# Kernel optimization log

Measured on AMD Instinct MI355X. Metric: run time of the kernel, lower is better.

The kernel has to match this reference:

```python
import jax, jax.numpy as jnp
import numpy as np

HIDDEN = 2048
N_HEADS = 16
N_KV = 2
HEAD_DIM = 256
PARTIAL = 0.25
ROT = int(HEAD_DIM * PARTIAL)  # 64
BATCH, SEQ = 1, 4096
NEG = -1e9


def apply_partial_rope(x, cos, sin):
    # x: (b, s, h, d); rotate first ROT dims (rotate-half convention), pass rest through.
    x_rot, x_pass = x[..., :ROT], x[..., ROT:]
    half = ROT // 2
    x1, x2 = x_rot[..., :half], x_rot[..., half:]
    c = cos[None, :, None, :]  # (1, s, 1, rot/2)
    s = sin[None, :, None, :]
    rotated = jnp.concatenate([x1 * c - x2 * s, x1 * s + x2 * c], axis=-1)
    return jnp.concatenate([rotated, x_pass], axis=-1)


def setup_inputs() -> dict:
    key = jax.random.key(0)
    ks = jax.random.split(key, 6)
    hidden_states = jax.random.normal(ks[0], (BATCH, SEQ, HIDDEN), dtype=jnp.float32)
    # RoPE tables: theta = 10000^{-2i/rot}
    inv_freq = 1.0 / (10000.0 ** (np.arange(0, ROT, 2, dtype=np.float32) / ROT))
    ang = np.arange(SEQ, dtype=np.float32)[:, None] * inv_freq[None, :]  # (s, rot/2)
    cos = jnp.asarray(np.cos(ang))
    sin = jnp.asarray(np.sin(ang))
    # causal mask (1,1,s,s)
    mask = jnp.triu(jnp.full((SEQ, SEQ), NEG, dtype=jnp.float32), k=1)[None, None]
    scale = 0.02
    wq = jax.random.normal(ks[1], (HIDDEN, N_HEADS * HEAD_DIM), dtype=jnp.float32) * scale
    wk = jax.random.normal(ks[2], (HIDDEN, N_KV * HEAD_DIM), dtype=jnp.float32) * scale
    wv = jax.random.normal(ks[3], (HIDDEN, N_KV * HEAD_DIM), dtype=jnp.float32) * scale
    wo = jax.random.normal(ks[4], (N_HEADS * HEAD_DIM, HIDDEN), dtype=jnp.float32) * scale
    return {"hidden_states": hidden_states, "cos": cos, "sin": sin,
            "attention_mask": mask, "wq": wq, "wk": wk, "wv": wv, "wo": wo}


def reference(hidden_states, cos, sin, attention_mask, wq, wk, wv, wo):
    b, s, _ = hidden_states.shape
    g = N_HEADS // N_KV
    scale = HEAD_DIM ** -0.5
    q = (hidden_states @ wq).reshape(b, s, N_HEADS, HEAD_DIM)
    k = (hidden_states @ wk).reshape(b, s, N_KV, HEAD_DIM)
    v = (hidden_states @ wv).reshape(b, s, N_KV, HEAD_DIM)
    q = apply_partial_rope(q, cos, sin)
    k = apply_partial_rope(k, cos, sin)
    new_k, new_v = k, v  # kv cache (no prior cache)
    # GQA without repeat_interleave: group q heads by their kv head.
    # repeat_interleave maps q head h -> kv head h // g, matching this reshape.
    qg = q.reshape(b, s, N_KV, g, HEAD_DIM)
    scores = jnp.einsum('bqkgd,blkd->bkgql', qg, k) * scale  # (b, kv, g, s, s)
    scores = scores + attention_mask[:, :, None]  # broadcast (b,1,1,s,s)
    probs = jax.nn.softmax(scores.astype(jnp.float32), axis=-1).astype(q.dtype)
    ctx = jnp.einsum('bkgql,blkd->bqkgd', probs, v)  # (b, s, kv, g, d)
    attn_out = ctx.reshape(b, s, N_HEADS * HEAD_DIM)
    output = attn_out @ wo
    return output, new_k, new_v
```

## Files before the change

kernel.cpp:

```cpp
#include <hip/hip_runtime.h>
#include <hip/hip_bf16.h>

typedef __bf16 bf16;
typedef bf16 bf16x8 __attribute__((ext_vector_type(8)));
typedef bf16 bf16x4 __attribute__((ext_vector_type(4)));
typedef float f32x4 __attribute__((ext_vector_type(4)));

#define SEQ    4096
#define HIDDEN 2048
#define NHEADS 16
#define NKV    2
#define HDIM   256
#define ROTD   64
#define ROTH   32
#define QN     (NHEADS*HDIM)
#define KVN    (NKV*HDIM)

typedef __attribute__((address_space(3))) unsigned int lds_u32;
typedef const __attribute__((address_space(1))) unsigned int glb_u32;
__device__ __forceinline__ void async_copy16(const void* g, void* l) {
  __builtin_amdgcn_global_load_lds((glb_u32*)g, (lds_u32*)l, 16, 0, 0);
}

__global__ __launch_bounds__(256) void convert_f32_bf16(
    const float* __restrict__ in, bf16* __restrict__ out, int n)
{
  int i = (blockIdx.x * 256 + threadIdx.x) * 4;
  if (i >= n) return;
  f32x4 v = *(const f32x4*)(in + i);
  bf16x4 o;
  #pragma unroll
  for (int j = 0; j < 4; j++) o[j] = (bf16)v[j];
  *(bf16x4*)(out + i) = o;
}

template<typename T>
__global__ __launch_bounds__(256) void transpose_to_bf16(
    const T* __restrict__ in, bf16* __restrict__ out, int R, int C)
{
  __shared__ float tile[32][33];
  int bx = blockIdx.x * 32;
  int by = blockIdx.y * 32;
  int tx = threadIdx.x & 31, ty = threadIdx.x >> 5;
  #pragma unroll
  for (int i = 0; i < 4; i++)
    tile[ty + i*8][tx] = (float)in[(size_t)(by + ty + i*8) * C + bx + tx];
  __syncthreads();
  #pragma unroll
  for (int i = 0; i < 4; i++)
    out[(size_t)(bx + ty + i*8) * R + by + tx] = (bf16)tile[tx][ty + i*8];
}

template<bool WF32, bool WBF16>
__global__ __launch_bounds__(256) void gemm_bt(
    const bf16* __restrict__ A, const bf16* __restrict__ Bt,
    float* __restrict__ Cf, bf16* __restrict__ Cb,
    int M, int N, int K)
{
  const int bm = blockIdx.y * 128;
  const int bn = blockIdx.x * 128;
  const int tid = threadIdx.x;
  const int wave = tid >> 6, lane = tid & 63;
  const int l16 = lane & 15, quad = lane >> 4;
  const int wr = (wave & 1) * 64;
  const int wc = (wave >> 1) * 64;

  __shared__ bf16 As[128*32];
  __shared__ bf16 Bs[128*32];

  f32x4 acc[4][4];
  #pragma unroll
  for (int r = 0; r < 4; r++)
    #pragma unroll
    for (int c = 0; c < 4; c++) acc[r][c] = (f32x4){0.f,0.f,0.f,0.f};

  const int arow = tid >> 2;
  const int acol = (tid & 3) * 8;
  const bf16* ag0 = A  + (size_t)(bm + arow)      * K + acol;
  const bf16* ag1 = A  + (size_t)(bm + 64 + arow) * K + acol;
  const bf16* bg0 = Bt + (size_t)(bn + arow)      * K + acol;
  const bf16* bg1 = Bt + (size_t)(bn + 64 + arow) * K + acol;
  bf16* la = As + tid*8;
  bf16* lb = Bs + tid*8;

  for (int kk = 0; kk < K; kk += 32) {
    __syncthreads();
    async_copy16(ag0 + kk, la);
    async_copy16(ag1 + kk, la + 2048);
    async_copy16(bg0 + kk, lb);
    async_copy16(bg1 + kk, lb + 2048);
    __syncthreads();

    bf16x8 af[4], bfr[4];
    #pragma unroll
    for (int r = 0; r < 4; r++) af[r]  = *(const bf16x8*)&As[(wr + r*16 + l16)*32 + quad*8];
    #pragma unroll
    for (int c = 0; c < 4; c++) bfr[c] = *(const bf16x8*)&Bs[(wc + c*16 + l16)*32 + quad*8];
    #pragma unroll
    for (int r = 0; r < 4; r++)
      #pragma unroll
      for (int c = 0; c < 4; c++)
        acc[r][c] = __builtin_amdgcn_mfma_f32_16x16x32_bf16(af[r], bfr[c], acc[r][c], 0, 0, 0);
  }

  #pragma unroll
  for (int r = 0; r < 4; r++)
    #pragma unroll
    for (int c = 0; c < 4; c++)
      #pragma unroll
      for (int rr = 0; rr < 4; rr++) {
        size_t idx = (size_t)(bm + wr + r*16 + quad*4 + rr) * N + bn + wc + c*16 + l16;
        if (WF32)  Cf[idx] = acc[r][c][rr];
        if (WBF16) Cb[idx] = (bf16)acc[r][c][rr];
      }
}

#define G256_STG(gp, stride, lbase, b, h, kt) do {                            \
    async_copy16((gp) + (size_t)((h)*128     ) * (stride) + (size_t)(kt)*64,  \
                 (lbase) + (b)*16384 + (h)*8192);                             \
    async_copy16((gp) + (size_t)((h)*128 + 64) * (stride) + (size_t)(kt)*64,  \
                 (lbase) + (b)*16384 + (h)*8192 + 4096);                      \
  } while (0)

#define G256_DSA(b, P) do {                                                   \
    _Pragma("unroll")                                                         \
    for (int m2 = 0; m2 < 2; m2++) {                                          \
      const int ro = (b)*16384 + arow0 + ((P)*2 + m2) * 1024;                 \
      af[m2][0] = *(const bf16x8*)&smem[ro + fc0];                            \
      af[m2][1] = *(const bf16x8*)&smem[ro + fc1];                            \
    }                                                                         \
  } while (0)

#define G256_DSB(b) do {                                                      \
    _Pragma("unroll")                                                         \
    for (int n4 = 0; n4 < 4; n4++) {                                          \
      const int ro = 32768 + (b)*16384 + brow0 + n4 * 1024;                   \
      bq[n4][0] = *(const bf16x8*)&smem[ro + fc0];                            \
      bq[n4][1] = *(const bf16x8*)&smem[ro + fc1];                            \
    }                                                                         \
  } while (0)

#define G256_MM(P) do {                                                       \
    _Pragma("unroll")                                                         \
    for (int m2 = 0; m2 < 2; m2++)                                            \
      _Pragma("unroll")                                                       \
      for (int n4 = 0; n4 < 4; n4++) {                                        \
        acc[(P)*2+m2][n4] = __builtin_amdgcn_mfma_f32_16x16x32_bf16(          \
            af[m2][0], bq[n4][0], acc[(P)*2+m2][n4], 0, 0, 0);                \
        acc[(P)*2+m2][n4] = __builtin_amdgcn_mfma_f32_16x16x32_bf16(          \
            af[m2][1], bq[n4][1], acc[(P)*2+m2][n4], 0, 0, 0);                \
      }                                                                       \
  } while (0)

#define G256_BAR  __builtin_amdgcn_s_barrier()
#define G256_WLG  do { asm volatile("s_waitcnt lgkmcnt(0)" ::: "memory");     \
                       __builtin_amdgcn_sched_barrier(0); } while (0)

template<bool WF32, bool WBF16>
__global__ __launch_bounds__(512, 2) void gemm256(
    const bf16* __restrict__ A, const bf16* __restrict__ Bt,
    float* __restrict__ Cf0, float* __restrict__ Cf1, bf16* __restrict__ Cb,
    int N, int K, int lda, int ldb)
{
  const int gx = gridDim.x;
  const int nwg = gx * gridDim.y;
  int wg = blockIdx.y * gx + blockIdx.x;
  wg = (wg & 7) * (nwg >> 3) + (wg >> 3);
  const int bn = (wg % gx) * 256;
  const int bm = (wg / gx) * 256;

  const int z = blockIdx.z;
  A  += (size_t)z * K;
  Bt += (size_t)z * K;
  float* __restrict__ Cf = z ? Cf1 : Cf0;

  const int tid = threadIdx.x;
  const int lane = tid & 63;
  const int l16 = lane & 15, quad = lane >> 4;
  const int wv = tid >> 6;
  const int wm = wv >> 2;
  const int wn = wv & 3;

  __shared__ bf16 smem[65536];

  const int srow = tid >> 3;
  const int scol = ((tid & 7) ^ (srow & 7)) << 3;
  const bf16* Ag = A  + (size_t)(bm + srow) * lda + scol;
  const bf16* Bg = Bt + (size_t)(bn + srow) * ldb + scol;
  bf16* lA = smem + tid * 8;
  bf16* lB = smem + 32768 + tid * 8;

  const int fsw = l16 & 7;
  const int fc0 = ((quad       ^ fsw) << 3);
  const int fc1 = (((4 + quad) ^ fsw) << 3);
  const int arow0 = (wm * 128 + l16) * 64;
  const int brow0 = (wn * 64  + l16) * 64;

  f32x4 acc[8][4];
  #pragma unroll
  for (int m = 0; m < 8; m++)
    #pragma unroll
    for (int n = 0; n < 4; n++) acc[m][n] = (f32x4){0.f,0.f,0.f,0.f};

  const int niter = K >> 7;

  G256_STG(Ag, lda, lA, 0, 0, 0);  G256_STG(Ag, lda, lA, 0, 1, 0);
  G256_STG(Bg, ldb, lB, 0, 0, 0);  G256_STG(Bg, ldb, lB, 0, 1, 0);
  G256_STG(Bg, ldb, lB, 1, 0, 1);  G256_STG(Bg, ldb, lB, 1, 1, 1);
  asm volatile("s_waitcnt vmcnt(4)" ::: "memory");
  G256_BAR;

  bf16x8 af[2][2];
  bf16x8 bq[4][2];

  for (int i = 0; i < niter; i++) {
    const int O = 2*i + 1;
    const bool nl = (i + 1 < niter);

    G256_DSB(0); G256_DSA(0, 0);
    G256_STG(Ag, lda, lA, 1, 0, O);
    G256_BAR; G256_WLG;
    __builtin_amdgcn_s_setprio(1); G256_MM(0); __builtin_amdgcn_s_setprio(0);
    G256_BAR;
    G256_DSA(0, 1);
    G256_STG(Ag, lda, lA, 1, 1, O);
    G256_BAR; G256_WLG;
    __builtin_amdgcn_s_setprio(1); G256_MM(1); __builtin_amdgcn_s_setprio(0);
    G256_BAR;
    G256_DSA(0, 2);
    if (nl) G256_STG(Bg, ldb, lB, 0, 0, O+1);
    G256_BAR; G256_WLG;
    __builtin_amdgcn_s_setprio(1); G256_MM(2); __builtin_amdgcn_s_setprio(0);
    G256_BAR;
    G256_DSA(0, 3);
    if (nl) G256_STG(Bg, ldb, lB, 0, 1, O+1);
    G256_BAR; G256_WLG;
    __builtin_amdgcn_s_setprio(1); G256_MM(3); __builtin_amdgcn_s_setprio(0);
    if (nl) asm volatile("s_waitcnt vmcnt(4)" ::: "memory");
    else    asm volatile("s_waitcnt vmcnt(0)" ::: "memory");
    G256_BAR;
    G256_DSB(1); G256_DSA(1, 0);
    if (nl) G256_STG(Ag, lda, lA, 0, 0, O+1);
    G256_BAR; G256_WLG;
    __builtin_amdgcn_s_setprio(1); G256_MM(0); __builtin_amdgcn_s_setprio(0);
    G256_BAR;
    G256_DSA(1, 1);
    if (nl) G256_STG(Ag, lda, lA, 0, 1, O+1);
    G256_BAR; G256_WLG;
    __builtin_amdgcn_s_setprio(1); G256_MM(1); __builtin_amdgcn_s_setprio(0);
    G256_BAR;
    G256_DSA(1, 2);
    if (nl) G256_STG(Bg, ldb, lB, 1, 0, O+2);
    G256_BAR; G256_WLG;
    __builtin_amdgcn_s_setprio(1); G256_MM(2); __builtin_amdgcn_s_setprio(0);
    G256_BAR;
    G256_DSA(1, 3);
    if (nl) G256_STG(Bg, ldb, lB, 1, 1, O+2);
    G256_BAR; G256_WLG;
    __builtin_amdgcn_s_setprio(1); G256_MM(3); __builtin_amdgcn_s_setprio(0);
    if (nl) asm volatile("s_waitcnt vmcnt(4)" ::: "memory");
    G256_BAR;
  }

  #pragma unroll
  for (int mf = 0; mf < 8; mf++)
    #pragma unroll
    for (int n = 0; n < 4; n++)
      #pragma unroll
      for (int rr = 0; rr < 4; rr++) {
        size_t idx = (size_t)(bm + wm*128 + mf*16 + quad*4 + rr) * N
                   + bn + wn*64 + n*16 + l16;
        if (WF32)  Cf[idx] = acc[mf][n][rr];
        if (WBF16) Cb[idx] = (bf16)acc[mf][n][rr];
      }
}

__global__ __launch_bounds__(256) void add_f32(
    const float* __restrict__ a, float* __restrict__ b, int n)
{
  int i = (blockIdx.x * 256 + threadIdx.x) * 4;
  if (i >= n) return;
  f32x4 x = *(const f32x4*)(a + i);
  f32x4 y = *(const f32x4*)(b + i);
  #pragma unroll
  for (int j = 0; j < 4; j++) y[j] += x[j];
  *(f32x4*)(b + i) = y;
}

__global__ __launch_bounds__(256) void rope_kernel(
    bf16* __restrict__ Q, bf16* __restrict__ K,
    const float* __restrict__ cosb, const float* __restrict__ sinb,
    float* __restrict__ newk)
{
  int s = blockIdx.x;
  int t = threadIdx.x;
  __shared__ float cf[ROTH], sf[ROTH];
  if (t < ROTH) { cf[t] = cosb[s*ROTH + t]; sf[t] = sinb[s*ROTH + t]; }
  __syncthreads();

  float qv[4];
  #pragma unroll
  for (int i = 0; i < 4; i++) {
    int w = t + 256*i;
    int h = w >> 6, d = w & 63;
    size_t base = ((size_t)s*NHEADS + h)*HDIM;
    if (d < ROTH) {
      float x1 = (float)Q[base + d], x2 = (float)Q[base + d + ROTH];
      qv[i] = x1*cf[d] - x2*sf[d];
    } else {
      int dd = d - ROTH;
      float x1 = (float)Q[base + dd], x2 = (float)Q[base + d];
      qv[i] = x1*sf[dd] + x2*cf[dd];
    }
  }
  float kvv[2];
  #pragma unroll
  for (int i = 0; i < 2; i++) {
    int w = t + 256*i;
    int h = w >> 8, d = w & 255;
    size_t base = ((size_t)s*NKV + h)*HDIM;
    if (d < ROTH) {
      kvv[i] = (float)K[base + d]*cf[d] - (float)K[base + d + ROTH]*sf[d];
    } else if (d < ROTD) {
      int dd = d - ROTH;
      kvv[i] = (float)K[base + dd]*sf[dd] + (float)K[base + d]*cf[dd];
    } else {
      kvv[i] = (float)K[base + d];
    }
  }
  __syncthreads();
  #pragma unroll
  for (int i = 0; i < 4; i++) {
    int w = t + 256*i;
    int h = w >> 6, d = w & 63;
    Q[((size_t)s*NHEADS + h)*HDIM + d] = (bf16)qv[i];
  }
  #pragma unroll
  for (int i = 0; i < 2; i++) {
    int w = t + 256*i;
    int h = w >> 8, d = w & 255;
    size_t base = ((size_t)s*NKV + h)*HDIM;
    K[base + d]    = (bf16)kvv[i];
    newk[base + d] = kvv[i];
  }
}

__global__ __launch_bounds__(256, 2) void attn_v6(
    const bf16* __restrict__ Q, const bf16* __restrict__ Kc,
    const bf16* __restrict__ Vt, bf16* __restrict__ ctx)
{
  const int d = blockIdx.y * gridDim.x + blockIdx.x;
  const int r = (d < 256) ? d : 767 - d;
  const int qs = 31 - (r >> 4);
  const int h  = r & 15, kvh = h >> 3;
  const int tid = threadIdx.x, wave = tid >> 6, lane = tid & 63;
  const int l16 = lane & 15, quad = lane >> 4;
  const int q0 = qs*128 + wave*32;

  __shared__ bf16 Ks[2][32*256];
  __shared__ bf16 Vs[2][256*32];
  __shared__ bf16 PsAll[4][32][40];
  bf16 (*Ps)[40] = PsAll[wave];

  bf16x8 aq[2][8];
  #pragma unroll
  for (int u = 0; u < 2; u++) {
    const bf16* qp = Q + (size_t)(q0 + u*16 + l16)*QN + h*HDIM + quad*8;
    #pragma unroll
    for (int c = 0; c < 8; c++) aq[u][c] = *(const bf16x8*)(qp + c*32);
  }

  f32x4 o[2][16];
  #pragma unroll
  for (int u = 0; u < 2; u++)
    #pragma unroll
    for (int c = 0; c < 16; c++) o[u][c] = (f32x4){0.f,0.f,0.f,0.f};
  float lsum[2][4] = {{0.f,0.f,0.f,0.f},{0.f,0.f,0.f,0.f}};

  const int krow0 = tid >> 5;
  const int kcg   = ((tid & 31) ^ (krow0 & 7)) * 8;
  const bf16* kg  = Kc + (size_t)kvh*HDIM + kcg;
  const int vd0 = tid >> 2;
  const int vcg = ((tid & 3) ^ (vd0 & 3)) * 8;
  const bf16* vg  = Vt + (size_t)(kvh*HDIM + vd0)*SEQ + vcg;

  const int ntiles = qs*4 + 4;

  #define ATTN_STAGE(t, b) do {                                               \
    const int _l0 = (t)*32;                                                   \
    bf16* _ks = &Ks[b][0] + tid*8;                                            \
    bf16* _vs = &Vs[b][0] + tid*8;                                            \
    _Pragma("unroll")                                                         \
    for (int p = 0; p < 4; p++) {                                             \
      async_copy16(kg + (size_t)(_l0 + p*8 + krow0)*KVN, _ks + p*2048);       \
      async_copy16(vg + (size_t)(p*64)*SEQ + _l0,        _vs + p*2048);       \
    }                                                                         \
  } while (0)

  ATTN_STAGE(0, 0);
  ATTN_STAGE(1, 1);
  asm volatile("s_waitcnt vmcnt(8)" ::: "memory");
  __builtin_amdgcn_s_barrier();

  for (int t = 0; t < ntiles; t++) {
    const int b  = t & 1;
    const int l0 = t*32;

    if (l0 <= q0 + 31) {
      f32x4 s[2][2];
      #pragma unroll
      for (int u = 0; u < 2; u++)
        #pragma unroll
        for (int t4 = 0; t4 < 2; t4++) s[u][t4] = (f32x4){0.f,0.f,0.f,0.f};
      #pragma unroll
      for (int c = 0; c < 8; c++) {
        const int cs = ((c*4 + quad) ^ (l16 & 7)) * 8;
        #pragma unroll
        for (int t4 = 0; t4 < 2; t4++) {
          bf16x8 kb = *(const bf16x8*)&Ks[b][(t4*16 + l16)*256 + cs];
          #pragma unroll
          for (int u = 0; u < 2; u++)
            s[u][t4] = __builtin_amdgcn_mfma_f32_16x16x32_bf16(aq[u][c], kb, s[u][t4], 0, 0, 0);
        }
      }

      const bool need_mask = (l0 + 31 > q0);
      #pragma unroll
      for (int u = 0; u < 2; u++)
        #pragma unroll
        for (int rr = 0; rr < 4; rr++) {
          const int row = q0 + u*16 + quad*4 + rr;
          float p0 = __expf(fmaf(s[u][0][rr], 0.0625f, -12.0f));
          float p1 = __expf(fmaf(s[u][1][rr], 0.0625f, -12.0f));
          if (need_mask) {
            if (l0 +      l16 > row) p0 = 0.f;
            if (l0 + 16 + l16 > row) p1 = 0.f;
          }
          lsum[u][rr] += p0 + p1;
          Ps[u*16 + quad*4 + rr][l16]      = (bf16)p0;
          Ps[u*16 + quad*4 + rr][16 + l16] = (bf16)p1;
        }

      bf16x8 pa[2];
      #pragma unroll
      for (int u = 0; u < 2; u++) pa[u] = *(const bf16x8*)&Ps[u*16 + l16][quad*8];
      #pragma unroll
      for (int c = 0; c < 16; c++) {
        const int vs = ((quad ^ (l16 & 3))) * 8;
        bf16x8 vb = *(const bf16x8*)&Vs[b][(c*16 + l16)*32 + vs];
        #pragma unroll
        for (int u = 0; u < 2; u++)
          o[u][c] = __builtin_amdgcn_mfma_f32_16x16x32_bf16(pa[u], vb, o[u][c], 0, 0, 0);
      }
    }

    if (t + 1 < ntiles) {
      __builtin_amdgcn_s_barrier();
      if (t + 2 < ntiles) {
        ATTN_STAGE(t + 2, b);
        asm volatile("s_waitcnt vmcnt(8)" ::: "memory");
      } else {
        asm volatile("s_waitcnt vmcnt(0)" ::: "memory");
      }
      __builtin_amdgcn_s_barrier();
    }
  }
  #undef ATTN_STAGE

  #pragma unroll
  for (int u = 0; u < 2; u++)
    #pragma unroll
    for (int rr = 0; rr < 4; rr++) {
      float l = lsum[u][rr];
      l += __shfl_xor(l, 1);
      l += __shfl_xor(l, 2);
      l += __shfl_xor(l, 4);
      l += __shfl_xor(l, 8);
      float inv = 1.0f / l;
      size_t base = (size_t)(q0 + u*16 + quad*4 + rr)*QN + h*HDIM;
      #pragma unroll
      for (int c = 0; c < 16; c++)
        ctx[base + c*16 + l16] = (bf16)(o[u][c][rr] * inv);
    }
}

extern "C" void kernel_launch(void* const* d_in, const int* in_sizes, int n_in,
                              void* d_out, int out_size, void* d_ws, size_t ws_size,
                              hipStream_t stream)
{
  const float* X    = (const float*)d_in[0];
  const float* cosb = (const float*)d_in[1];
  const float* sinb = (const float*)d_in[2];
  const float* wq   = (const float*)d_in[4];
  const float* wk   = (const float*)d_in[5];
  const float* wv   = (const float*)d_in[6];
  const float* wo   = (const float*)d_in[7];

  float* out  = (float*)d_out;
  float* newk = out  + (size_t)SEQ*HIDDEN;
  float* newv = newk + (size_t)SEQ*KVN;

  bf16* Xb  = (bf16*)d_ws;
  bf16* wqT = Xb  + (size_t)SEQ*HIDDEN;
  bf16* Qb  = wqT + (size_t)QN*HIDDEN;
  bf16* Kb  = Qb  + (size_t)SEQ*QN;
  bf16* Vb  = Kb  + (size_t)SEQ*KVN;
  bf16* Vt  = Vb  + (size_t)SEQ*KVN;
  bf16* wkT = Vt  + (size_t)KVN*SEQ;
  bf16* wvT = wkT + (size_t)KVN*HIDDEN;
  bf16* woT = wvT + (size_t)KVN*HIDDEN;
  bf16* ctx = Xb;
  float* part = (float*)Qb;

  dim3 blk(256);
  convert_f32_bf16<<<dim3(SEQ*HIDDEN/1024), blk, 0, stream>>>(X, Xb, SEQ*HIDDEN);
  transpose_to_bf16<float><<<dim3(QN/32,     HIDDEN/32), blk, 0, stream>>>(wq, wqT, HIDDEN, QN);
  transpose_to_bf16<float><<<dim3(KVN/32,    HIDDEN/32), blk, 0, stream>>>(wk, wkT, HIDDEN, KVN);
  transpose_to_bf16<float><<<dim3(KVN/32,    HIDDEN/32), blk, 0, stream>>>(wv, wvT, HIDDEN, KVN);
  transpose_to_bf16<float><<<dim3(HIDDEN/32, QN/32),     blk, 0, stream>>>(wo, woT, QN, HIDDEN);

  gemm256<false,true><<<dim3(QN/256, SEQ/256, 1), dim3(512), 0, stream>>>(
      Xb, wqT, nullptr, nullptr, Qb, QN, HIDDEN, HIDDEN, HIDDEN);
  gemm_bt<false,true><<<dim3(KVN/128, SEQ/128), blk, 0, stream>>>(Xb, wkT, nullptr, Kb, SEQ, KVN, HIDDEN);
  gemm_bt<true, true><<<dim3(KVN/128, SEQ/128), blk, 0, stream>>>(Xb, wvT, newv,   Vb, SEQ, KVN, HIDDEN);

  rope_kernel<<<dim3(SEQ), blk, 0, stream>>>(Qb, Kb, cosb, sinb, newk);
  transpose_to_bf16<bf16><<<dim3(KVN/32, SEQ/32), blk, 0, stream>>>(Vb, Vt, SEQ, KVN);

  attn_v6<<<dim3(SEQ/128, NHEADS), blk, 0, stream>>>(Qb, Kb, Vt, ctx);

  gemm256<true,false><<<dim3(HIDDEN/256, SEQ/256, 2), dim3(512), 0, stream>>>(
      ctx, woT, out, part, nullptr, HIDDEN, QN/2, QN, QN);
  add_f32<<<dim3(SEQ*HIDDEN/1024), blk, 0, stream>>>(part, out, SEQ*HIDDEN);
}
```

Baseline: 722.6 us.

## Share K/V tiles across two heads per 512-thread attention block with 64-key tiles

The attention kernel now runs 8 waves per block covering two query heads that share one KV head, so each K/V tile loaded into LDS serves twice as many query rows. Key tiles grow from 32 to 64 rows and each is processed in two 32-key halves. It also switches exp to exp2 with a folded scale constant and raises wave priority around the MFMA loops. The aim is to halve global K/V traffic and the number of barriers per key, at the cost of larger LDS use (64KB+), lower occupancy per block, and dropping the heavy-first load-balancing block order.

```diff
diff --git a/kernel.cpp b/kernel.cpp
--- a/kernel.cpp
+++ b/kernel.cpp
@@ -345,21 +345,21 @@
   }
 }
 
-__global__ __launch_bounds__(256, 2) void attn_v6(
+__global__ __launch_bounds__(512, 2) void attn_v7(
     const bf16* __restrict__ Q, const bf16* __restrict__ Kc,
     const bf16* __restrict__ Vt, bf16* __restrict__ ctx)
 {
-  const int d = blockIdx.y * gridDim.x + blockIdx.x;
-  const int r = (d < 256) ? d : 767 - d;
-  const int qs = 31 - (r >> 4);
-  const int h  = r & 15, kvh = h >> 3;
+  const int qs  = blockIdx.x;
+  const int hp  = blockIdx.y;
+  const int kvh = hp >> 2;
   const int tid = threadIdx.x, wave = tid >> 6, lane = tid & 63;
   const int l16 = lane & 15, quad = lane >> 4;
-  const int q0 = qs*128 + wave*32;
-
-  __shared__ bf16 Ks[2][32*256];
-  __shared__ bf16 Vs[2][256*32];
-  __shared__ bf16 PsAll[4][32][40];
+  const int h   = hp*2 + (wave >> 2);
+  const int q0  = qs*128 + (wave & 3)*32;
+
+  __shared__ bf16 Ks[2][64*256];
+  __shared__ bf16 Vs[2][256*64];
+  __shared__ bf16 PsAll[8][32][40];
   bf16 (*Ps)[40] = PsAll[wave];
 
   bf16x8 aq[2][8];
@@ -380,20 +380,20 @@
   const int krow0 = tid >> 5;
   const int kcg   = ((tid & 31) ^ (krow0 & 7)) * 8;
   const bf16* kg  = Kc + (size_t)kvh*HDIM + kcg;
-  const int vd0 = tid >> 2;
-  const int vcg = ((tid & 3) ^ (vd0 & 3)) * 8;
+  const int vd0 = tid >> 3;
+  const int vcg = ((tid & 7) ^ (vd0 & 7)) * 8;
   const bf16* vg  = Vt + (size_t)(kvh*HDIM + vd0)*SEQ + vcg;
 
-  const int ntiles = qs*4 + 4;
+  const int ntiles = qs*2 + 2;
 
   #define ATTN_STAGE(t, b) do {                                               \
-    const int _l0 = (t)*32;                                                   \
+    const int _l0 = (t)*64;                                                   \
     bf16* _ks = &Ks[b][0] + tid*8;                                            \
     bf16* _vs = &Vs[b][0] + tid*8;                                            \
     _Pragma("unroll")                                                         \
     for (int p = 0; p < 4; p++) {                                             \
-      async_copy16(kg + (size_t)(_l0 + p*8 + krow0)*KVN, _ks + p*2048);       \
-      async_copy16(vg + (size_t)(p*64)*SEQ + _l0,        _vs + p*2048);       \
+      async_copy16(kg + (size_t)(_l0 + p*16 + krow0)*KVN, _ks + p*4096);      \
+      async_copy16(vg + (size_t)(p*64)*SEQ + _l0,         _vs + p*4096);      \
     }                                                                         \
   } while (0)
 
@@ -402,55 +402,66 @@
   asm volatile("s_waitcnt vmcnt(8)" ::: "memory");
   __builtin_amdgcn_s_barrier();
 
+  const float C1 = 0.09016844f;
+  const float C0 = -17.31234050f;
+
   for (int t = 0; t < ntiles; t++) {
     const int b  = t & 1;
-    const int l0 = t*32;
-
-    if (l0 <= q0 + 31) {
-      f32x4 s[2][2];
-      #pragma unroll
-      for (int u = 0; u < 2; u++)
+    const int l0 = t*64;
+
+    #pragma unroll
+    for (int hh = 0; hh < 2; hh++) {
+      const int l0h = l0 + hh*32;
+      if (l0h <= q0 + 31) {
+        f32x4 s2[2][2];
         #pragma unroll
-        for (int t4 = 0; t4 < 2; t4++) s[u][t4] = (f32x4){0.f,0.f,0.f,0.f};
-      #pragma unroll
-      for (int c = 0; c < 8; c++) {
-        const int cs = ((c*4 + quad) ^ (l16 & 7)) * 8;
+        for (int u = 0; u < 2; u++)
+          #pragma unroll
+          for (int t4 = 0; t4 < 2; t4++) s2[u][t4] = (f32x4){0.f,0.f,0.f,0.f};
+        __builtin_amdgcn_s_setprio(1);
         #pragma unroll
-        for (int t4 = 0; t4 < 2; t4++) {
-          bf16x8 kb = *(const bf16x8*)&Ks[b][(t4*16 + l16)*256 + cs];
+        for (int c = 0; c < 8; c++) {
+          const int cs = ((c*4 + quad) ^ (l16 & 7)) * 8;
+          #pragma unroll
+          for (int t4 = 0; t4 < 2; t4++) {
+            bf16x8 kb = *(const bf16x8*)&Ks[b][(hh*32 + t4*16 + l16)*256 + cs];
+            #pragma unroll
+            for (int u = 0; u < 2; u++)
+              s2[u][t4] = __builtin_amdgcn_mfma_f32_16x16x32_bf16(aq[u][c], kb, s2[u][t4], 0, 0, 0);
+          }
+        }
+        __builtin_amdgcn_s_setprio(0);
+
+        const bool need_mask = (l0h + 31 > q0);
+        #pragma unroll
+        for (int u = 0; u < 2; u++)
+          #pragma unroll
+          for (int rr = 0; rr < 4; rr++) {
+            const int row = q0 + u*16 + quad*4 + rr;
+            float p0 = exp2f(fmaf(s2[u][0][rr], C1, C0));
+            float p1 = exp2f(fmaf(s2[u][1][rr], C1, C0));
+            if (need_mask) {
+              if (l0h +      l16 > row) p0 = 0.f;
+              if (l0h + 16 + l16 > row) p1 = 0.f;
+            }
+            lsum[u][rr] += p0 + p1;
+            Ps[u*16 + quad*4 + rr][l16]      = (bf16)p0;
+            Ps[u*16 + quad*4 + rr][16 + l16] = (bf16)p1;
+          }
+
+        bf16x8 pa[2];
+        #pragma unroll
+        for (int u = 0; u < 2; u++) pa[u] = *(const bf16x8*)&Ps[u*16 + l16][quad*8];
+        const int vs = (((hh*4 + quad) ^ (l16 & 7))) * 8;
+        __builtin_amdgcn_s_setprio(1);
+        #pragma unroll
+        for (int c = 0; c < 16; c++) {
+          bf16x8 vb = *(const bf16x8*)&Vs[b][(c*16 + l16)*64 + vs];
           #pragma unroll
           for (int u = 0; u < 2; u++)
-            s[u][t4] = __builtin_amdgcn_mfma_f32_16x16x32_bf16(aq[u][c], kb, s[u][t4], 0, 0, 0);
+            o[u][c] = __builtin_amdgcn_mfma_f32_16x16x32_bf16(pa[u], vb, o[u][c], 0, 0, 0);
         }
-      }
-
-      const bool need_mask = (l0 + 31 > q0);
-      #pragma unroll
-      for (int u = 0; u < 2; u++)
-        #pragma unroll
-        for (int rr = 0; rr < 4; rr++) {
-          const int row = q0 + u*16 + quad*4 + rr;
-          float p0 = __expf(fmaf(s[u][0][rr], 0.0625f, -12.0f));
-          float p1 = __expf(fmaf(s[u][1][rr], 0.0625f, -12.0f));
-          if (need_mask) {
-            if (l0 +      l16 > row) p0 = 0.f;
-            if (l0 + 16 + l16 > row) p1 = 0.f;
-          }
-          lsum[u][rr] += p0 + p1;
-          Ps[u*16 + quad*4 + rr][l16]      = (bf16)p0;
-          Ps[u*16 + quad*4 + rr][16 + l16] = (bf16)p1;
-        }
-
-      bf16x8 pa[2];
-      #pragma unroll
-      for (int u = 0; u < 2; u++) pa[u] = *(const bf16x8*)&Ps[u*16 + l16][quad*8];
-      #pragma unroll
-      for (int c = 0; c < 16; c++) {
-        const int vs = ((quad ^ (l16 & 3))) * 8;
-        bf16x8 vb = *(const bf16x8*)&Vs[b][(c*16 + l16)*32 + vs];
-        #pragma unroll
-        for (int u = 0; u < 2; u++)
-          o[u][c] = __builtin_amdgcn_mfma_f32_16x16x32_bf16(pa[u], vb, o[u][c], 0, 0, 0);
+        __builtin_amdgcn_s_setprio(0);
       }
     }
 
@@ -527,7 +538,7 @@
   rope_kernel<<<dim3(SEQ), blk, 0, stream>>>(Qb, Kb, cosb, sinb, newk);
   transpose_to_bf16<bf16><<<dim3(KVN/32, SEQ/32), blk, 0, stream>>>(Vb, Vt, SEQ, KVN);
 
-  attn_v6<<<dim3(SEQ/128, NHEADS), blk, 0, stream>>>(Qb, Kb, Vt, ctx);
+  attn_v7<<<dim3(SEQ/128, NHEADS/2), dim3(512), 0, stream>>>(Qb, Kb, Vt, ctx);
 
   gemm256<true,false><<<dim3(HIDDEN/256, SEQ/256, 2), dim3(512), 0, stream>>>(
       ctx, woT, out, part, nullptr, HIDDEN, QN/2, QN, QN);
```

Result: slower. 738.7 us (+2.2%).
